# Kernel tuning notes

Measured on AMD Instinct MI355X. Metric: run time of the kernel, lower is better.

## Reference

```python
import jax, jax.numpy as jnp
import numpy as np

N_HEADS = 1

def setup_inputs() -> dict:
    key = jax.random.key(0)
    kq, kk, kv = jax.random.split(key, 3)
    B, G, H, S = 16, 32, 32, 4096  # batch, n_var (groups), hidden_dim, seq_len
    q = jax.random.normal(kq, (B, G, H, S), dtype=jnp.float32)
    k = jax.random.normal(kk, (B, G, H, S), dtype=jnp.float32)
    v = jax.random.normal(kv, (B, G, H, S), dtype=jnp.float32)
    return {"q": q, "k": k, "v": v}

def reference(q, k, v):
    # q, k, v: (B, G, hidden_dim, S); n_heads = 1 as used by TAMCaD_T
    B, Gq, hidden, S = q.shape
    Gkv = k.shape[1]
    nh = N_HEADS
    dk = hidden // nh
    scale = dk ** -0.5
    qr = q.reshape(B, Gq, nh, dk, S)
    kr = k.reshape(B, Gkv, nh, dk, S)
    vr = v.reshape(B, Gkv, nh, dk, S)
    # logits: (B, nh, S, Gq, Gkv) -- attention over variable pairs per timestep
    logits = scale * jnp.einsum('bghds,bfhds->bhsgf', qr, kr)
    attn = jax.nn.softmax(logits, axis=-1)
    # x: (B, nh, S, Gq, dk)
    x = jnp.einsum('bhsgf,bfhds->bhsgd', attn, vr)
    # permute (0,3,1,4,2) -> (B, Gq, nh, dk, S) -> (B, Gq*nh*dk, S)
    x = x.transpose(0, 3, 1, 4, 2).reshape(B, Gq * nh * dk, S)
    # attentions/logits: mean over heads, then (B, Gq, Gkv, S)
    attentions = attn.mean(axis=1).transpose(0, 2, 3, 1)
    attention_logits = logits.mean(axis=1).transpose(0, 2, 3, 1)
    return x, attentions, attention_logits
```

## Files before the change

### kernel.cpp

```cpp
#include <hip/hip_runtime.h>


constexpr int S_LEN = 4096;
constexpr int GG = 32;
constexpr int HH = 32;
constexpr int TS = 16;
constexpr float SCALE = 0.17677669529663687f;

__device__ __forceinline__ unsigned bf16pack(float a, float b) {
    unsigned ua = __float_as_uint(a);
    unsigned ub = __float_as_uint(b);
    ua = (ua + 0x7fffu + ((ua >> 16) & 1u)) >> 16;
    ub = (ub + 0x7fffu + ((ub >> 16) & 1u)) >> 16;
    return ua | (ub << 16);
}

__global__ __launch_bounds__(512, 4) void tamcad_fused(
    const float* __restrict__ q, const float* __restrict__ k,
    const float* __restrict__ v, float* __restrict__ x_out,
    float* __restrict__ attn_out, float* __restrict__ logit_out)
{
    __shared__ __align__(16) unsigned lds[GG * TS * 16 * 2];

    const int nwg = gridDim.x;
    const int cpx = nwg >> 3;
    const int raw = blockIdx.x;
    const int logical = (raw & 7) * cpx + (raw >> 3);
    const int b  = logical >> 8;
    const int st = logical & 255;
    const int s0 = st * TS;

    const int tid = threadIdx.x;
    const int g = tid >> 4;
    const int s = tid & 15;

    const int baseB = b * (GG * HH);
    const float* qb = q + (size_t)baseB * S_LEN + s0;
    const float* kb = k + (size_t)baseB * S_LEN + s0;
    const float* vb = v + (size_t)baseB * S_LEN + s0;

    float qreg[32];
    #pragma unroll
    for (int d = 0; d < 32; ++d)
        qreg[d] = qb[(size_t)(g * HH + d) * S_LEN + s];

    {
        const int fst = g;
        const int dp  = s;
        const int dpl = dp & 3;
        const int dph = (dp >> 2) << 2;
        unsigned* const wbase = &lds[fst * 256 + dpl];
        unsigned* const was[4] = { wbase + (dph ^ 0),  wbase + (dph ^ 4),
                                   wbase + (dph ^ 8),  wbase + (dph ^ 12) };

        const float4* k0p = reinterpret_cast<const float4*>(kb + (size_t)(fst * HH + 2 * dp)     * S_LEN);
        const float4* k1p = reinterpret_cast<const float4*>(kb + (size_t)(fst * HH + 2 * dp + 1) * S_LEN);
        const float4* v0p = reinterpret_cast<const float4*>(vb + (size_t)(fst * HH + 2 * dp)     * S_LEN);
        const float4* v1p = reinterpret_cast<const float4*>(vb + (size_t)(fst * HH + 2 * dp + 1) * S_LEN);

        float r0[16], r1[16], t0[16], t1[16];
        #pragma unroll
        for (int sq = 0; sq < 4; ++sq) {
            *reinterpret_cast<float4*>(&r0[sq * 4]) = k0p[sq];
            *reinterpret_cast<float4*>(&r1[sq * 4]) = k1p[sq];
            *reinterpret_cast<float4*>(&t0[sq * 4]) = v0p[sq];
            *reinterpret_cast<float4*>(&t1[sq * 4]) = v1p[sq];
        }
        #pragma unroll
        for (int ss = 0; ss < 16; ++ss) {
            unsigned* wp = was[(ss >> 1) & 3] + ss * 16;
            wp[0]    = bf16pack(r0[ss], r1[ss]);
            wp[8192] = bf16pack(t0[ss], t1[ss]);
        }
    }
    __syncthreads();

    const int xs = (s >> 1) & 3;
    const unsigned* const rp0 = &lds[s * 16 + ((0 ^ xs) << 2)];
    const unsigned* const rp1 = &lds[s * 16 + ((1 ^ xs) << 2)];
    const unsigned* const rp2 = &lds[s * 16 + ((2 ^ xs) << 2)];
    const unsigned* const rp3 = &lds[s * 16 + ((3 ^ xs) << 2)];

    float l[32];
#define QKW(u, d0) { \
        const float klo_ = __uint_as_float((u) << 16); \
        const float khi_ = __uint_as_float((u) & 0xffff0000u); \
        a0 = fmaf(qreg[d0], klo_, a0); \
        a1 = fmaf(qreg[(d0) + 1], khi_, a1); }
    #pragma unroll
    for (int f = 0; f < 32; ++f) {
        float a0 = 0.f, a1 = 0.f;
        const uint4 c0 = *reinterpret_cast<const uint4*>(rp0 + f * 256);
        const uint4 c1 = *reinterpret_cast<const uint4*>(rp1 + f * 256);
        const uint4 c2 = *reinterpret_cast<const uint4*>(rp2 + f * 256);
        const uint4 c3 = *reinterpret_cast<const uint4*>(rp3 + f * 256);
        QKW(c0.x,  0) QKW(c0.y,  2) QKW(c0.z,  4) QKW(c0.w,  6)
        QKW(c1.x,  8) QKW(c1.y, 10) QKW(c1.z, 12) QKW(c1.w, 14)
        QKW(c2.x, 16) QKW(c2.y, 18) QKW(c2.z, 20) QKW(c2.w, 22)
        QKW(c3.x, 24) QKW(c3.y, 26) QKW(c3.z, 28) QKW(c3.w, 30)
        l[f] = (a0 + a1) * SCALE;
        logit_out[(size_t)(baseB + g * GG + f) * S_LEN + s0 + s] = l[f];
    }
#undef QKW

    float tm[16];
    #pragma unroll
    for (int i = 0; i < 16; ++i) tm[i] = fmaxf(l[2 * i], l[2 * i + 1]);
    #pragma unroll
    for (int i = 0; i < 8; ++i) tm[i] = fmaxf(tm[i], tm[i + 8]);
    #pragma unroll
    for (int i = 0; i < 4; ++i) tm[i] = fmaxf(tm[i], tm[i + 4]);
    const float m = fmaxf(fmaxf(tm[0], tm[1]), fmaxf(tm[2], tm[3]));

    float ts4[4] = {0.f, 0.f, 0.f, 0.f};
    #pragma unroll
    for (int f = 0; f < 32; ++f) {
        l[f] = __expf(l[f] - m);
        ts4[f & 3] += l[f];
    }
    const float sum = (ts4[0] + ts4[1]) + (ts4[2] + ts4[3]);
    const float inv = __builtin_amdgcn_rcpf(sum);
    #pragma unroll
    for (int f = 0; f < 32; ++f) {
        l[f] *= inv;
        attn_out[(size_t)(baseB + g * GG + f) * S_LEN + s0 + s] = l[f];
    }

    float xa[32];
    #pragma unroll
    for (int d = 0; d < 32; ++d) xa[d] = 0.f;
#define PVW(u, d0) { \
        const float vlo_ = __uint_as_float((u) << 16); \
        const float vhi_ = __uint_as_float((u) & 0xffff0000u); \
        xa[d0] = fmaf(av, vlo_, xa[d0]); \
        xa[(d0) + 1] = fmaf(av, vhi_, xa[(d0) + 1]); }
    #pragma unroll
    for (int f = 0; f < 32; ++f) {
        const float av = l[f];
        const uint4 c0 = *reinterpret_cast<const uint4*>(rp0 + 8192 + f * 256);
        const uint4 c1 = *reinterpret_cast<const uint4*>(rp1 + 8192 + f * 256);
        const uint4 c2 = *reinterpret_cast<const uint4*>(rp2 + 8192 + f * 256);
        const uint4 c3 = *reinterpret_cast<const uint4*>(rp3 + 8192 + f * 256);
        PVW(c0.x,  0) PVW(c0.y,  2) PVW(c0.z,  4) PVW(c0.w,  6)
        PVW(c1.x,  8) PVW(c1.y, 10) PVW(c1.z, 12) PVW(c1.w, 14)
        PVW(c2.x, 16) PVW(c2.y, 18) PVW(c2.z, 20) PVW(c2.w, 22)
        PVW(c3.x, 24) PVW(c3.y, 26) PVW(c3.z, 28) PVW(c3.w, 30)
    }
#undef PVW
    #pragma unroll
    for (int d = 0; d < 32; ++d)
        x_out[(size_t)(baseB + g * HH + d) * S_LEN + s0 + s] = xa[d];
}

extern "C" void kernel_launch(void* const* d_in, const int* in_sizes, int n_in,
                              void* d_out, int out_size, void* d_ws, size_t ws_size,
                              hipStream_t stream) {
    const float* q = (const float*)d_in[0];
    const float* k = (const float*)d_in[1];
    const float* v = (const float*)d_in[2];
    float* out = (float*)d_out;
    const int n = in_sizes[0];
    const int B = n / (GG * HH * S_LEN);
    float* x_out     = out;
    float* attn_out  = out + (size_t)n;
    float* logit_out = out + (size_t)2 * n;
    const int nwg = B * (S_LEN / TS);
    tamcad_fused<<<dim3(nwg), dim3(512), 0, stream>>>(q, k, v, x_out, attn_out, logit_out);
}
```

Measured before the change: 535.9 us.

## Double tile width, reuse one LDS buffer for K then V, split register halves

Doubles the sequence tile to 32 with 1024-thread blocks. A single LDS buffer is reused: K is staged first, then V is staged into the same space after an extra barrier. The q registers and x accumulators are split into two 16-wide halves, aiming to cut register pressure and raise occupancy. The cost is an extra barrier, V loads serialized after the softmax, and q loaded in two phases.

```diff
diff --git a/kernel.cpp b/kernel.cpp
--- a/kernel.cpp
+++ b/kernel.cpp
@@ -4,7 +4,7 @@
 constexpr int S_LEN = 4096;
 constexpr int GG = 32;
 constexpr int HH = 32;
-constexpr int TS = 16;
+constexpr int TS = 32;
 constexpr float SCALE = 0.17677669529663687f;
 
 __device__ __forceinline__ unsigned bf16pack(float a, float b) {
@@ -15,64 +15,62 @@
     return ua | (ub << 16);
 }
 
-__global__ __launch_bounds__(512, 4) void tamcad_fused(
+__global__ __launch_bounds__(1024, 8) void tamcad_fused(
     const float* __restrict__ q, const float* __restrict__ k,
     const float* __restrict__ v, float* __restrict__ x_out,
     float* __restrict__ attn_out, float* __restrict__ logit_out)
 {
-    __shared__ __align__(16) unsigned lds[GG * TS * 16 * 2];
+    __shared__ __align__(16) unsigned lds[GG * TS * 16];
 
     const int nwg = gridDim.x;
     const int cpx = nwg >> 3;
     const int raw = blockIdx.x;
     const int logical = (raw & 7) * cpx + (raw >> 3);
-    const int b  = logical >> 8;
-    const int st = logical & 255;
+    const int b  = logical >> 7;
+    const int st = logical & 127;
     const int s0 = st * TS;
 
     const int tid = threadIdx.x;
-    const int g = tid >> 4;
-    const int s = tid & 15;
+    const int g = tid >> 5;
+    const int s = tid & 31;
+
+    const int fst = tid >> 5;
+    const int dp  = (tid >> 1) & 15;
+    const int sh  = tid & 1;
+    const int dpl = dp & 3;
+    const int dph = dp & 12;
 
     const int baseB = b * (GG * HH);
     const float* qb = q + (size_t)baseB * S_LEN + s0;
     const float* kb = k + (size_t)baseB * S_LEN + s0;
     const float* vb = v + (size_t)baseB * S_LEN + s0;
 
-    float qreg[32];
+#define STAGE(SRC) do { \
+    const float* r0_ = (SRC) + (size_t)(fst * HH + 2 * dp) * S_LEN + sh * 16; \
+    const float* r1_ = r0_ + S_LEN; \
+    unsigned* const lb_ = &lds[fst * 512 + dpl]; \
+    _Pragma("unroll") \
+    for (int sq_ = 0; sq_ < 4; ++sq_) { \
+        const float4 a4_ = *reinterpret_cast<const float4*>(r0_ + sq_ * 4); \
+        const float4 b4_ = *reinterpret_cast<const float4*>(r1_ + sq_ * 4); \
+        const float al_[4] = {a4_.x, a4_.y, a4_.z, a4_.w}; \
+        const float bl_[4] = {b4_.x, b4_.y, b4_.z, b4_.w}; \
+        _Pragma("unroll") \
+        for (int e_ = 0; e_ < 4; e_ += 2) { \
+            const int s_  = sh * 16 + sq_ * 4 + e_; \
+            const int xs_ = (s_ >> 1) & 3; \
+            unsigned* wp_ = lb_ + s_ * 16 + (dph ^ (xs_ << 2)); \
+            wp_[0]  = bf16pack(al_[e_],     bl_[e_]); \
+            wp_[16] = bf16pack(al_[e_ + 1], bl_[e_ + 1]); \
+        } \
+    } \
+} while (0)
+
+    STAGE(kb);
+    float qr[16];
     #pragma unroll
-    for (int d = 0; d < 32; ++d)
-        qreg[d] = qb[(size_t)(g * HH + d) * S_LEN + s];
-
-    {
-        const int fst = g;
-        const int dp  = s;
-        const int dpl = dp & 3;
-        const int dph = (dp >> 2) << 2;
-        unsigned* const wbase = &lds[fst * 256 + dpl];
-        unsigned* const was[4] = { wbase + (dph ^ 0),  wbase + (dph ^ 4),
-                                   wbase + (dph ^ 8),  wbase + (dph ^ 12) };
-
-        const float4* k0p = reinterpret_cast<const float4*>(kb + (size_t)(fst * HH + 2 * dp)     * S_LEN);
-        const float4* k1p = reinterpret_cast<const float4*>(kb + (size_t)(fst * HH + 2 * dp + 1) * S_LEN);
-        const float4* v0p = reinterpret_cast<const float4*>(vb + (size_t)(fst * HH + 2 * dp)     * S_LEN);
-        const float4* v1p = reinterpret_cast<const float4*>(vb + (size_t)(fst * HH + 2 * dp + 1) * S_LEN);
-
-        float r0[16], r1[16], t0[16], t1[16];
-        #pragma unroll
-        for (int sq = 0; sq < 4; ++sq) {
-            *reinterpret_cast<float4*>(&r0[sq * 4]) = k0p[sq];
-            *reinterpret_cast<float4*>(&r1[sq * 4]) = k1p[sq];
-            *reinterpret_cast<float4*>(&t0[sq * 4]) = v0p[sq];
-            *reinterpret_cast<float4*>(&t1[sq * 4]) = v1p[sq];
-        }
-        #pragma unroll
-        for (int ss = 0; ss < 16; ++ss) {
-            unsigned* wp = was[(ss >> 1) & 3] + ss * 16;
-            wp[0]    = bf16pack(r0[ss], r1[ss]);
-            wp[8192] = bf16pack(t0[ss], t1[ss]);
-        }
-    }
+    for (int d = 0; d < 16; ++d)
+        qr[d] = qb[(size_t)(g * HH + d) * S_LEN + s];
     __syncthreads();
 
     const int xs = (s >> 1) & 3;
@@ -81,75 +79,105 @@
     const unsigned* const rp2 = &lds[s * 16 + ((2 ^ xs) << 2)];
     const unsigned* const rp3 = &lds[s * 16 + ((3 ^ xs) << 2)];
 
-    float l[32];
 #define QKW(u, d0) { \
         const float klo_ = __uint_as_float((u) << 16); \
         const float khi_ = __uint_as_float((u) & 0xffff0000u); \
-        a0 = fmaf(qreg[d0], klo_, a0); \
-        a1 = fmaf(qreg[(d0) + 1], khi_, a1); }
+        a0 = fmaf(qr[d0], klo_, a0); \
+        a1 = fmaf(qr[(d0) + 1], khi_, a1); }
+
+    float l[32];
     #pragma unroll
     for (int f = 0; f < 32; ++f) {
+        const uint4 c0 = *reinterpret_cast<const uint4*>(rp0 + f * 512);
+        const uint4 c1 = *reinterpret_cast<const uint4*>(rp1 + f * 512);
         float a0 = 0.f, a1 = 0.f;
-        const uint4 c0 = *reinterpret_cast<const uint4*>(rp0 + f * 256);
-        const uint4 c1 = *reinterpret_cast<const uint4*>(rp1 + f * 256);
-        const uint4 c2 = *reinterpret_cast<const uint4*>(rp2 + f * 256);
-        const uint4 c3 = *reinterpret_cast<const uint4*>(rp3 + f * 256);
         QKW(c0.x,  0) QKW(c0.y,  2) QKW(c0.z,  4) QKW(c0.w,  6)
         QKW(c1.x,  8) QKW(c1.y, 10) QKW(c1.z, 12) QKW(c1.w, 14)
-        QKW(c2.x, 16) QKW(c2.y, 18) QKW(c2.z, 20) QKW(c2.w, 22)
-        QKW(c3.x, 24) QKW(c3.y, 26) QKW(c3.z, 28) QKW(c3.w, 30)
-        l[f] = (a0 + a1) * SCALE;
+        l[f] = a0 + a1;
+    }
+    #pragma unroll
+    for (int d = 0; d < 16; ++d)
+        qr[d] = qb[(size_t)(g * HH + 16 + d) * S_LEN + s];
+    #pragma unroll
+    for (int f = 0; f < 32; ++f) {
+        const uint4 c2 = *reinterpret_cast<const uint4*>(rp2 + f * 512);
+        const uint4 c3 = *reinterpret_cast<const uint4*>(rp3 + f * 512);
+        float a0 = 0.f, a1 = 0.f;
+        QKW(c2.x,  0) QKW(c2.y,  2) QKW(c2.z,  4) QKW(c2.w,  6)
+        QKW(c3.x,  8) QKW(c3.y, 10) QKW(c3.z, 12) QKW(c3.w, 14)
+        l[f] = (l[f] + a0 + a1) * SCALE;
         logit_out[(size_t)(baseB + g * GG + f) * S_LEN + s0 + s] = l[f];
     }
 #undef QKW
 
-    float tm[16];
-    #pragma unroll
-    for (int i = 0; i < 16; ++i) tm[i] = fmaxf(l[2 * i], l[2 * i + 1]);
-    #pragma unroll
-    for (int i = 0; i < 8; ++i) tm[i] = fmaxf(tm[i], tm[i + 8]);
-    #pragma unroll
-    for (int i = 0; i < 4; ++i) tm[i] = fmaxf(tm[i], tm[i + 4]);
-    const float m = fmaxf(fmaxf(tm[0], tm[1]), fmaxf(tm[2], tm[3]));
-
-    float ts4[4] = {0.f, 0.f, 0.f, 0.f};
-    #pragma unroll
-    for (int f = 0; f < 32; ++f) {
-        l[f] = __expf(l[f] - m);
-        ts4[f & 3] += l[f];
-    }
-    const float sum = (ts4[0] + ts4[1]) + (ts4[2] + ts4[3]);
-    const float inv = __builtin_amdgcn_rcpf(sum);
-    #pragma unroll
-    for (int f = 0; f < 32; ++f) {
-        l[f] *= inv;
-        attn_out[(size_t)(baseB + g * GG + f) * S_LEN + s0 + s] = l[f];
+    {
+        float tm[16];
+        #pragma unroll
+        for (int i = 0; i < 16; ++i) tm[i] = fmaxf(l[2 * i], l[2 * i + 1]);
+        #pragma unroll
+        for (int i = 0; i < 8; ++i) tm[i] = fmaxf(tm[i], tm[i + 8]);
+        #pragma unroll
+        for (int i = 0; i < 4; ++i) tm[i] = fmaxf(tm[i], tm[i + 4]);
+        const float m = fmaxf(fmaxf(tm[0], tm[1]), fmaxf(tm[2], tm[3]));
+        float ts4[4] = {0.f, 0.f, 0.f, 0.f};
+        #pragma unroll
+        for (int f = 0; f < 32; ++f) {
+            l[f] = __expf(l[f] - m);
+            ts4[f & 3] += l[f];
+        }
+        const float sum = (ts4[0] + ts4[1]) + (ts4[2] + ts4[3]);
+        const float inv = __builtin_amdgcn_rcpf(sum);
+        #pragma unroll
+        for (int f = 0; f < 32; ++f) {
+            l[f] *= inv;
+            attn_out[(size_t)(baseB + g * GG + f) * S_LEN + s0 + s] = l[f];
+        }
     }
 
-    float xa[32];
-    #pragma unroll
-    for (int d = 0; d < 32; ++d) xa[d] = 0.f;
+    __syncthreads();
+    STAGE(vb);
+    __syncthreads();
+
 #define PVW(u, d0) { \
         const float vlo_ = __uint_as_float((u) << 16); \
         const float vhi_ = __uint_as_float((u) & 0xffff0000u); \
         xa[d0] = fmaf(av, vlo_, xa[d0]); \
         xa[(d0) + 1] = fmaf(av, vhi_, xa[(d0) + 1]); }
-    #pragma unroll
-    for (int f = 0; f < 32; ++f) {
-        const float av = l[f];
-        const uint4 c0 = *reinterpret_cast<const uint4*>(rp0 + 8192 + f * 256);
-        const uint4 c1 = *reinterpret_cast<const uint4*>(rp1 + 8192 + f * 256);
-        const uint4 c2 = *reinterpret_cast<const uint4*>(rp2 + 8192 + f * 256);
-        const uint4 c3 = *reinterpret_cast<const uint4*>(rp3 + 8192 + f * 256);
-        PVW(c0.x,  0) PVW(c0.y,  2) PVW(c0.z,  4) PVW(c0.w,  6)
-        PVW(c1.x,  8) PVW(c1.y, 10) PVW(c1.z, 12) PVW(c1.w, 14)
-        PVW(c2.x, 16) PVW(c2.y, 18) PVW(c2.z, 20) PVW(c2.w, 22)
-        PVW(c3.x, 24) PVW(c3.y, 26) PVW(c3.z, 28) PVW(c3.w, 30)
+
+    {
+        float xa[16];
+        #pragma unroll
+        for (int d = 0; d < 16; ++d) xa[d] = 0.f;
+        #pragma unroll
+        for (int f = 0; f < 32; ++f) {
+            const float av = l[f];
+            const uint4 c0 = *reinterpret_cast<const uint4*>(rp0 + f * 512);
+            const uint4 c1 = *reinterpret_cast<const uint4*>(rp1 + f * 512);
+            PVW(c0.x,  0) PVW(c0.y,  2) PVW(c0.z,  4) PVW(c0.w,  6)
+            PVW(c1.x,  8) PVW(c1.y, 10) PVW(c1.z, 12) PVW(c1.w, 14)
+        }
+        #pragma unroll
+        for (int d = 0; d < 16; ++d)
+            x_out[(size_t)(baseB + g * HH + d) * S_LEN + s0 + s] = xa[d];
+    }
+    {
+        float xa[16];
+        #pragma unroll
+        for (int d = 0; d < 16; ++d) xa[d] = 0.f;
+        #pragma unroll
+        for (int f = 0; f < 32; ++f) {
+            const float av = l[f];
+            const uint4 c2 = *reinterpret_cast<const uint4*>(rp2 + f * 512);
+            const uint4 c3 = *reinterpret_cast<const uint4*>(rp3 + f * 512);
+            PVW(c2.x,  0) PVW(c2.y,  2) PVW(c2.z,  4) PVW(c2.w,  6)
+            PVW(c3.x,  8) PVW(c3.y, 10) PVW(c3.z, 12) PVW(c3.w, 14)
+        }
+        #pragma unroll
+        for (int d = 0; d < 16; ++d)
+            x_out[(size_t)(baseB + g * HH + 16 + d) * S_LEN + s0 + s] = xa[d];
     }
 #undef PVW
-    #pragma unroll
-    for (int d = 0; d < 32; ++d)
-        x_out[(size_t)(baseB + g * HH + d) * S_LEN + s0 + s] = xa[d];
+#undef STAGE
 }
 
 extern "C" void kernel_launch(void* const* d_in, const int* in_sizes, int n_in,
@@ -165,5 +193,5 @@
     float* attn_out  = out + (size_t)n;
     float* logit_out = out + (size_t)2 * n;
     const int nwg = B * (S_LEN / TS);
-    tamcad_fused<<<dim3(nwg), dim3(512), 0, stream>>>(q, k, v, x_out, attn_out, logit_out);
+    tamcad_fused<<<dim3(nwg), dim3(1024), 0, stream>>>(q, k, v, x_out, attn_out, logit_out);
 }
```

Result: slower. 838.5 us (+56.5%).
